# Kernel optimization log

Hardware: AMD Instinct MI355X
Metric: run time of the kernel (lower is better)

## Reference

```python
import jax, jax.numpy as jnp
import numpy as np

EMBED = 1024
HEADS = 16
HEAD = EMBED // HEADS
B, S = 8, 1024


def setup_inputs() -> dict:
    key = jax.random.key(0)
    ks = jax.random.split(key, 12)
    inp = {
        "values": jax.random.normal(ks[0], (B, S, EMBED), jnp.float32),
        "keys": jax.random.normal(ks[1], (B, S, EMBED), jnp.float32),
        "query": jax.random.normal(ks[2], (B, S, EMBED), jnp.float32),
        # causal mask broadcastable to [B, heads, q, k]
        "mask": jnp.broadcast_to(jnp.tril(jnp.ones((S, S), jnp.int32))[None, None], (B, 1, S, S)),
        "Wv": jax.random.normal(ks[3], (HEAD, HEAD), jnp.float32) / np.sqrt(HEAD),
        "bv": jnp.zeros((HEAD,), jnp.float32),
        "Wk": jax.random.normal(ks[4], (HEAD, HEAD), jnp.float32) / np.sqrt(HEAD),
        "bk": jnp.zeros((HEAD,), jnp.float32),
        "Wq": jax.random.normal(ks[5], (HEAD, HEAD), jnp.float32) / np.sqrt(HEAD),
        "bq": jnp.zeros((HEAD,), jnp.float32),
        "Wfc": jax.random.normal(ks[6], (EMBED, EMBED), jnp.float32) / np.sqrt(EMBED),
        "bfc": jnp.zeros((EMBED,), jnp.float32),
    }
    return inp


def reference(values, keys, query, mask, Wv, bv, Wk, bk, Wq, bq, Wfc, bfc):
    N, q_len = query.shape[0], query.shape[1]
    k_len, v_len = keys.shape[1], values.shape[1]
    # split heads: [N, S, H, D]
    v = values.reshape(N, v_len, HEADS, HEAD)
    k = keys.reshape(N, k_len, HEADS, HEAD)
    q = query.reshape(N, q_len, HEADS, HEAD)
    # per-head linear projections (torch Linear: x @ W.T + b)
    v = v @ Wv.T + bv
    k = k @ Wk.T + bk
    q = q @ Wq.T + bq
    # scores [N, H, q, k]
    scores = jnp.einsum('nqhz,nkhz->nhqk', q, k)
    scores = jnp.where(mask == 0, -jnp.inf, scores)
    # NOTE: original divides by sqrt(query_size) (sequence length), not head dim
    attn = jax.nn.softmax(scores / jnp.sqrt(jnp.float32(q_len)), axis=-1)
    out = jnp.einsum('nhqk,nkhz->nqhz', attn, v).reshape(N, q_len, HEADS * HEAD)
    return out @ Wfc.T + bfc
```

## Files before the change

kernel.cpp:

```cpp
#include <hip/hip_runtime.h>
#include <stdint.h>

typedef __attribute__((ext_vector_type(8))) short short8;
typedef __attribute__((ext_vector_type(4))) short short4v;
typedef __attribute__((ext_vector_type(4))) float floatx4;
typedef __attribute__((ext_vector_type(4))) unsigned short ushort4v;

#define HEADS 16
#define HEAD 64
#define SEQ 1024
#define BATCH 8

__device__ __forceinline__ unsigned short f2bf(float f) {
    union { float f; unsigned int u; } v; v.f = f;
    unsigned int r = v.u + 0x7FFFu + ((v.u >> 16) & 1u);
    return (unsigned short)(r >> 16);
}

__device__ __forceinline__ void gload_lds16(const void* g, void* l) {
    __builtin_amdgcn_global_load_lds((const __attribute__((address_space(1))) void*)g,
                                     (__attribute__((address_space(3))) void*)l, 16, 0, 0);
}

__global__ __launch_bounds__(256) void cvt_kernel(const float* __restrict__ in,
                                                  unsigned short* __restrict__ out) {
    int i = (blockIdx.x * 256 + threadIdx.x) * 4;
    float4 f = *(const float4*)(in + i);
    ushort4v v;
    v.x = f2bf(f.x); v.y = f2bf(f.y); v.z = f2bf(f.z); v.w = f2bf(f.w);
    *(ushort4v*)(out + i) = v;
}

__global__ __launch_bounds__(256) void proj_qk_kernel(
    const float* __restrict__ Qin, const float* __restrict__ Kin,
    const float* __restrict__ Wq, const float* __restrict__ bq,
    const float* __restrict__ Wk, const float* __restrict__ bk,
    unsigned short* __restrict__ q_ws, unsigned short* __restrict__ k_ws)
{
    const int tid = threadIdx.x;
    const int wave = tid >> 6, lane = tid & 63;
    const int lq = lane & 15, quad = lane >> 4;
    const int proj = blockIdx.y;

    const float* X = proj ? Kin : Qin;
    const float* W = proj ? Wk : Wq;
    const float* bias = proj ? bk : bq;
    unsigned short* dstb = proj ? k_ws : q_ws;

    const int gr0 = blockIdx.x * 16;
    const int h0 = wave * 4;
    const int b = gr0 >> 10, s0 = gr0 & 1023;

    __shared__ unsigned short sT[4][16 * 68];

    short8 wf[4][2];
#pragma unroll
    for (int nt = 0; nt < 4; ++nt) {
        const float* wr = W + (nt * 16 + lq) * 64 + quad * 8;
#pragma unroll
        for (int ks = 0; ks < 2; ++ks) {
            float4 f0 = *(const float4*)(wr + ks * 32);
            float4 f1 = *(const float4*)(wr + ks * 32 + 4);
            short8 v;
            v[0] = (short)f2bf(f0.x); v[1] = (short)f2bf(f0.y);
            v[2] = (short)f2bf(f0.z); v[3] = (short)f2bf(f0.w);
            v[4] = (short)f2bf(f1.x); v[5] = (short)f2bf(f1.y);
            v[6] = (short)f2bf(f1.z); v[7] = (short)f2bf(f1.w);
            wf[nt][ks] = v;
        }
    }

    float bqk[4];
#pragma unroll
    for (int nt = 0; nt < 4; ++nt) bqk[nt] = bias[nt * 16 + lq];
    const float qscale = 0.03125f * 1.44269504088896340736f;
    const float oscale = proj ? 1.0f : qscale;

    const float* xb = X + (size_t)(gr0 + lq) * 1024 + quad * 8;
    const floatx4 zero4 = {0.f, 0.f, 0.f, 0.f};

    unsigned short* tw = &sT[wave][0];
    const unsigned short* tr = &sT[wave][(lane >> 2) * 68 + (lane & 3) * 16];

    float4 xf[4];
    { const float* p = xb + h0 * 64;
      xf[0] = *(const float4*)p;        xf[1] = *(const float4*)(p + 4);
      xf[2] = *(const float4*)(p + 32); xf[3] = *(const float4*)(p + 36); }
#pragma unroll
    for (int hh = 0; hh < 4; ++hh) {
        float4 xn[4];
        if (hh < 3) {
            const float* p = xb + (h0 + hh + 1) * 64;
            xn[0] = *(const float4*)p;        xn[1] = *(const float4*)(p + 4);
            xn[2] = *(const float4*)(p + 32); xn[3] = *(const float4*)(p + 36);
        }
        short8 aq[2];
#pragma unroll
        for (int ks = 0; ks < 2; ++ks) {
            short8 a;
            a[0] = (short)f2bf(xf[ks * 2].x);     a[1] = (short)f2bf(xf[ks * 2].y);
            a[2] = (short)f2bf(xf[ks * 2].z);     a[3] = (short)f2bf(xf[ks * 2].w);
            a[4] = (short)f2bf(xf[ks * 2 + 1].x); a[5] = (short)f2bf(xf[ks * 2 + 1].y);
            a[6] = (short)f2bf(xf[ks * 2 + 1].z); a[7] = (short)f2bf(xf[ks * 2 + 1].w);
            aq[ks] = a;
        }
        floatx4 acc[4] = {zero4, zero4, zero4, zero4};
#pragma unroll
        for (int ks = 0; ks < 2; ++ks)
#pragma unroll
            for (int nt = 0; nt < 4; ++nt)
                acc[nt] = __builtin_amdgcn_mfma_f32_16x16x32_bf16(aq[ks], wf[nt][ks], acc[nt], 0, 0, 0);

#pragma unroll
        for (int nt = 0; nt < 4; ++nt)
#pragma unroll
            for (int r = 0; r < 4; ++r)
                tw[(quad * 4 + r) * 68 + nt * 16 + lq] = f2bf((acc[nt][r] + bqk[nt]) * oscale);

        short8 o0 = *(const short8*)tr;
        short8 o1 = *(const short8*)(tr + 8);
        unsigned short* dst = dstb + ((size_t)((b * 16 + h0 + hh) * 1024) + s0) * 64 + lane * 16;
        *(short8*)dst = o0;
        *(short8*)(dst + 8) = o1;

#pragma unroll
        for (int i = 0; i < 4; ++i) xf[i] = xn[i];
    }
}

__global__ __launch_bounds__(256) void proj_v_kernel(
    const float* __restrict__ Vin,
    const float* __restrict__ Wv, const float* __restrict__ bv,
    unsigned short* __restrict__ v_ws)
{
    const int tid = threadIdx.x;
    const int wave = tid >> 6, lane = tid & 63;
    const int lq = lane & 15, quad = lane >> 4;

    const int gr0 = blockIdx.x * 16;
    const int h0 = wave * 4;
    const int b = gr0 >> 10, s0 = gr0 & 1023;

    __shared__ unsigned short sT[4][64 * 20];

    short8 wf[4][2];
#pragma unroll
    for (int nt = 0; nt < 4; ++nt) {
        const float* wr = Wv + (nt * 16 + lq) * 64 + quad * 8;
#pragma unroll
        for (int ks = 0; ks < 2; ++ks) {
            float4 f0 = *(const float4*)(wr + ks * 32);
            float4 f1 = *(const float4*)(wr + ks * 32 + 4);
            short8 v;
            v[0] = (short)f2bf(f0.x); v[1] = (short)f2bf(f0.y);
            v[2] = (short)f2bf(f0.z); v[3] = (short)f2bf(f0.w);
            v[4] = (short)f2bf(f1.x); v[5] = (short)f2bf(f1.y);
            v[6] = (short)f2bf(f1.z); v[7] = (short)f2bf(f1.w);
            wf[nt][ks] = v;
        }
    }

    float bvr[4][4];
#pragma unroll
    for (int nt = 0; nt < 4; ++nt)
#pragma unroll
        for (int r = 0; r < 4; ++r) bvr[nt][r] = bv[nt * 16 + quad * 4 + r];

    const float* xb = Vin + (size_t)(gr0 + lq) * 1024 + quad * 8;
    const floatx4 zero4 = {0.f, 0.f, 0.f, 0.f};

    unsigned short* tw = &sT[wave][0];
    const int rrow = lane >> 1, rhalf = lane & 1;
    const unsigned short* tr0 = &sT[wave][rrow * 20 + rhalf * 8];
    const unsigned short* tr1 = &sT[wave][(rrow + 32) * 20 + rhalf * 8];

    float4 xf[4];
    { const float* p = xb + h0 * 64;
      xf[0] = *(const float4*)p;        xf[1] = *(const float4*)(p + 4);
      xf[2] = *(const float4*)(p + 32); xf[3] = *(const float4*)(p + 36); }
#pragma unroll
    for (int hh = 0; hh < 4; ++hh) {
        float4 xn[4];
        if (hh < 3) {
            const float* p = xb + (h0 + hh + 1) * 64;
            xn[0] = *(const float4*)p;        xn[1] = *(const float4*)(p + 4);
            xn[2] = *(const float4*)(p + 32); xn[3] = *(const float4*)(p + 36);
        }
        short8 aq[2];
#pragma unroll
        for (int ks = 0; ks < 2; ++ks) {
            short8 a;
            a[0] = (short)f2bf(xf[ks * 2].x);     a[1] = (short)f2bf(xf[ks * 2].y);
            a[2] = (short)f2bf(xf[ks * 2].z);     a[3] = (short)f2bf(xf[ks * 2].w);
            a[4] = (short)f2bf(xf[ks * 2 + 1].x); a[5] = (short)f2bf(xf[ks * 2 + 1].y);
            a[6] = (short)f2bf(xf[ks * 2 + 1].z); a[7] = (short)f2bf(xf[ks * 2 + 1].w);
            aq[ks] = a;
        }
        floatx4 acc[4] = {zero4, zero4, zero4, zero4};
#pragma unroll
        for (int ks = 0; ks < 2; ++ks)
#pragma unroll
            for (int nt = 0; nt < 4; ++nt)
                acc[nt] = __builtin_amdgcn_mfma_f32_16x16x32_bf16(wf[nt][ks], aq[ks], acc[nt], 0, 0, 0);

#pragma unroll
        for (int nt = 0; nt < 4; ++nt)
#pragma unroll
            for (int r = 0; r < 4; ++r)
                tw[(nt * 16 + quad * 4 + r) * 20 + lq] = f2bf(acc[nt][r] + bvr[nt][r]);

        short8 o0 = *(const short8*)tr0;
        short8 o1 = *(const short8*)tr1;
        unsigned short* vh = v_ws + (size_t)((b * 16 + h0 + hh) * 64) * 1024 + s0 + rhalf * 8;
        *(short8*)(vh + (size_t)rrow * 1024) = o0;
        *(short8*)(vh + (size_t)(rrow + 32) * 1024) = o1;

#pragma unroll
        for (int i = 0; i < 4; ++i) xf[i] = xn[i];
    }
}

__global__ __launch_bounds__(256, 2) void attn_kernel(
    const unsigned short* __restrict__ q_ws, const unsigned short* __restrict__ k_ws,
    const unsigned short* __restrict__ v_ws, unsigned short* __restrict__ attn_ws)
{
    const int bh = blockIdx.x;
    const int b = bh >> 4, h = bh & 15;
    const int tid = threadIdx.x;
    const int wave = tid >> 6, lane = tid & 63;
    const int lq = lane & 15, quad = lane >> 4;
    const int r8 = lane >> 3, ch = lane & 7;
    const int sw = ch ^ r8;

    __shared__ unsigned short sK[64 * 64];
    __shared__ unsigned short sV[64 * 64];
    __shared__ unsigned short sP[4][32 * 64];

    const size_t head_off = (size_t)bh * SEQ * HEAD;
    const unsigned short* qb = q_ws + head_off;
    const unsigned short* kb = k_ws + head_off;
    const unsigned short* vb = v_ws + head_off;

    short8 ones;
#pragma unroll
    for (int j = 0; j < 8; ++j) ones[j] = (short)0x3F80;

    const floatx4 zero4 = {0.f, 0.f, 0.f, 0.f};

    for (int pass = 0; pass < 2; ++pass) {
        const int qt = pass ? (7 - blockIdx.y) : blockIdx.y;
        const int q0 = qt * 128;
        const int q_lo = q0 + wave * 32;
        const int q_hi = q_lo + 31;
        const int nkt = 2 * qt + 2;

        short8 aq[2][2];
#pragma unroll
        for (int rg = 0; rg < 2; ++rg) {
            const unsigned short* qp = qb + (size_t)(q0 + wave * 32 + rg * 16 + lq) * 64 + quad * 8;
            aq[rg][0] = *(const short8*)qp;
            aq[rg][1] = *(const short8*)(qp + 32);
        }

        floatx4 o[2][4];
        floatx4 lacc[2] = {zero4, zero4};
#pragma unroll
        for (int rg = 0; rg < 2; ++rg)
#pragma unroll
            for (int nt = 0; nt < 4; ++nt) o[rg][nt] = zero4;

        for (int kt = 0; kt < nkt; ++kt) {
#pragma unroll
            for (int i = 0; i < 2; ++i) {
                int br = wave * 16 + i * 8;
                const char* gK = (const char*)(kb + (size_t)(kt * 64 + br + r8) * 64) + sw * 16;
                gload_lds16(gK, (char*)sK + br * 128);
                const char* gV = (const char*)(vb + (size_t)(br + r8) * 1024 + kt * 64) + sw * 16;
                gload_lds16(gV, (char*)sV + br * 128);
            }
            __syncthreads();

            const bool skip = (kt * 64 > q_hi);
            if (!skip) {
                const bool full = (kt * 64 + 63 <= q_lo);

                floatx4 s[2][4];
#pragma unroll
                for (int rg = 0; rg < 2; ++rg)
#pragma unroll
                    for (int nt = 0; nt < 4; ++nt) s[rg][nt] = zero4;
#pragma unroll
                for (int ks = 0; ks < 2; ++ks) {
#pragma unroll
                    for (int nt = 0; nt < 4; ++nt) {
                        short8 kf = *(const short8*)(sK + (nt * 16 + lq) * 64 +
                                                     (((quad + 4 * ks) ^ (lq & 7)) * 8));
                        s[0][nt] = __builtin_amdgcn_mfma_f32_16x16x32_bf16(aq[0][ks], kf, s[0][nt], 0, 0, 0);
                        s[1][nt] = __builtin_amdgcn_mfma_f32_16x16x32_bf16(aq[1][ks], kf, s[1][nt], 0, 0, 0);
                    }
                }

                unsigned short* wp = &sP[wave][0];
#pragma unroll
                for (int rg = 0; rg < 2; ++rg) {
#pragma unroll
                    for (int nt = 0; nt < 4; ++nt) {
                        int kcol = kt * 64 + nt * 16 + lq;
                        int chn = (((nt * 2 + (lq >> 3)) ^ (quad << 1)) * 8) + (lq & 7);
#pragma unroll
                        for (int r = 0; r < 4; ++r) {
                            float p = __builtin_amdgcn_exp2f(s[rg][nt][r]);
                            if (!full) {
                                int qrow = q_lo + rg * 16 + quad * 4 + r;
                                if (kcol > qrow) p = 0.f;
                            }
                            wp[(rg * 16 + quad * 4 + r) * 64 + chn] = f2bf(p);
                        }
                    }
                }

                short8 vf[4][2];
#pragma unroll
                for (int nt = 0; nt < 4; ++nt)
#pragma unroll
                    for (int ks = 0; ks < 2; ++ks)
                        vf[nt][ks] = *(const short8*)(sV + (nt * 16 + lq) * 64 +
                                                      (((quad + 4 * ks) ^ (lq & 7)) * 8));
#pragma unroll
                for (int rg = 0; rg < 2; ++rg) {
#pragma unroll
                    for (int ks = 0; ks < 2; ++ks) {
                        short8 pa = *(const short8*)&sP[wave][(rg * 16 + lq) * 64 +
                                     (((ks * 4 + quad) ^ (((lq >> 2) & 3) << 1)) * 8)];
                        lacc[rg] = __builtin_amdgcn_mfma_f32_16x16x32_bf16(pa, ones, lacc[rg], 0, 0, 0);
#pragma unroll
                        for (int nt = 0; nt < 4; ++nt)
                            o[rg][nt] = __builtin_amdgcn_mfma_f32_16x16x32_bf16(pa, vf[nt][ks], o[rg][nt], 0, 0, 0);
                    }
                }
            }
            __syncthreads();
        }

#pragma unroll
        for (int rg = 0; rg < 2; ++rg) {
            float inv[4];
#pragma unroll
            for (int r = 0; r < 4; ++r) inv[r] = 1.f / lacc[rg][r];
            const int srow_base = q0 + wave * 32 + rg * 16 + quad * 4;
#pragma unroll
            for (int nt = 0; nt < 4; ++nt) {
                int col = h * 64 + nt * 16 + lq;
#pragma unroll
                for (int r = 0; r < 4; ++r) {
                    attn_ws[((size_t)(b * SEQ + srow_base + r)) * 1024 + col] = f2bf(o[rg][nt][r] * inv[r]);
                }
            }
        }
    }
}

__global__ __launch_bounds__(256) void fc_kernel(
    const unsigned short* __restrict__ A, const unsigned short* __restrict__ Bw,
    const float* __restrict__ bias, float* __restrict__ out)
{
    const int nt0 = blockIdx.x * 128;
    const int mt0 = blockIdx.y * 128;
    const int tid = threadIdx.x;
    const int wave = tid >> 6, lane = tid & 63;
    const int lq = lane & 15, quad = lane >> 4;
    const int wm = (wave >> 1) * 64, wn = (wave & 1) * 64;

    __shared__ unsigned short sA[128 * 32];
    __shared__ unsigned short sB[128 * 32];

    const floatx4 zero4 = {0.f, 0.f, 0.f, 0.f};
    floatx4 acc[4][4];
#pragma unroll
    for (int i = 0; i < 4; ++i)
#pragma unroll
        for (int j = 0; j < 4; ++j) acc[i][j] = zero4;

    for (int kt = 0; kt < 32; ++kt) {
#pragma unroll
        for (int issue = 0; issue < 2; ++issue) {
            int off = (issue * 4 + wave) * 1024 + lane * 16;
            int row = off >> 6;
            int cb = off & 63;
            const char* ga = (const char*)A + (size_t)(mt0 + row) * 2048 + kt * 64 + cb;
            gload_lds16(ga, (char*)sA + (issue * 4 + wave) * 1024);
            const char* gb = (const char*)Bw + (size_t)(nt0 + row) * 2048 + kt * 64 + cb;
            gload_lds16(gb, (char*)sB + (issue * 4 + wave) * 1024);
        }
        __syncthreads();

        short8 af[4], bf[4];
#pragma unroll
        for (int i = 0; i < 4; ++i) {
            af[i] = *(const short8*)(sA + (wm + i * 16 + lq) * 32 + quad * 8);
            bf[i] = *(const short8*)(sB + (wn + i * 16 + lq) * 32 + quad * 8);
        }
#pragma unroll
        for (int mi = 0; mi < 4; ++mi)
#pragma unroll
            for (int ni = 0; ni < 4; ++ni)
                acc[mi][ni] = __builtin_amdgcn_mfma_f32_16x16x32_bf16(af[mi], bf[ni], acc[mi][ni], 0, 0, 0);
        __syncthreads();
    }

#pragma unroll
    for (int mi = 0; mi < 4; ++mi) {
#pragma unroll
        for (int ni = 0; ni < 4; ++ni) {
            int col = nt0 + wn + ni * 16 + lq;
            float bc = bias[col];
#pragma unroll
            for (int r = 0; r < 4; ++r) {
                int row = mt0 + wm + mi * 16 + quad * 4 + r;
                out[(size_t)row * 1024 + col] = acc[mi][ni][r] + bc;
            }
        }
    }
}

extern "C" void kernel_launch(void* const* d_in, const int* in_sizes, int n_in,
                              void* d_out, int out_size, void* d_ws, size_t ws_size,
                              hipStream_t stream)
{
    const float* values = (const float*)d_in[0];
    const float* keys   = (const float*)d_in[1];
    const float* query  = (const float*)d_in[2];
    const float* Wv  = (const float*)d_in[4];
    const float* bv  = (const float*)d_in[5];
    const float* Wk  = (const float*)d_in[6];
    const float* bk  = (const float*)d_in[7];
    const float* Wq  = (const float*)d_in[8];
    const float* bq  = (const float*)d_in[9];
    const float* Wfc = (const float*)d_in[10];
    const float* bfc = (const float*)d_in[11];
    float* out = (float*)d_out;

    char* ws = (char*)d_ws;
    unsigned short* q_ws    = (unsigned short*)(ws);
    unsigned short* k_ws    = (unsigned short*)(ws + (16u << 20));
    unsigned short* v_ws    = (unsigned short*)(ws + (32u << 20));
    unsigned short* attn_ws = (unsigned short*)(ws + (48u << 20));
    unsigned short* wfc_ws  = (unsigned short*)(ws + (64u << 20));

    cvt_kernel<<<dim3(1024), dim3(256), 0, stream>>>(Wfc, wfc_ws);
    proj_qk_kernel<<<dim3(512, 2), dim3(256), 0, stream>>>(
        query, keys, Wq, bq, Wk, bk, q_ws, k_ws);
    proj_v_kernel<<<dim3(512), dim3(256), 0, stream>>>(values, Wv, bv, v_ws);
    attn_kernel<<<dim3(128, 4), dim3(256), 0, stream>>>(q_ws, k_ws, v_ws, attn_ws);
    fc_kernel<<<dim3(8, 64), dim3(256), 0, stream>>>(attn_ws, wfc_ws, bfc, out);
}
```

Before: 262.6 us.

## Fuse Wfc conversion into V projection, split attention grid, deepen FC K-tile

Folds the Wfc fp32-to-bf16 conversion into proj_v_kernel, which removes one kernel launch. The attention kernel drops its two-pass balanced q-tile pairing in favour of one q-tile per block on an 8-wide grid, and raises the launch-bounds occupancy hint to 4. The FC GEMM moves to a 64-wide K tile with an XOR-swizzled LDS layout, which halves the number of loop iterations and barriers. The risks are causal load imbalance across attention blocks and extra register pressure from the higher occupancy target.

```diff
diff --git a/kernel.cpp b/kernel.cpp
--- a/kernel.cpp
+++ b/kernel.cpp
@@ -2,7 +2,6 @@
 #include <stdint.h>
 
 typedef __attribute__((ext_vector_type(8))) short short8;
-typedef __attribute__((ext_vector_type(4))) short short4v;
 typedef __attribute__((ext_vector_type(4))) float floatx4;
 typedef __attribute__((ext_vector_type(4))) unsigned short ushort4v;
 
@@ -20,15 +19,6 @@
 __device__ __forceinline__ void gload_lds16(const void* g, void* l) {
     __builtin_amdgcn_global_load_lds((const __attribute__((address_space(1))) void*)g,
                                      (__attribute__((address_space(3))) void*)l, 16, 0, 0);
-}
-
-__global__ __launch_bounds__(256) void cvt_kernel(const float* __restrict__ in,
-                                                  unsigned short* __restrict__ out) {
-    int i = (blockIdx.x * 256 + threadIdx.x) * 4;
-    float4 f = *(const float4*)(in + i);
-    ushort4v v;
-    v.x = f2bf(f.x); v.y = f2bf(f.y); v.z = f2bf(f.z); v.w = f2bf(f.w);
-    *(ushort4v*)(out + i) = v;
 }
 
 __global__ __launch_bounds__(256) void proj_qk_kernel(
@@ -131,11 +121,23 @@
 __global__ __launch_bounds__(256) void proj_v_kernel(
     const float* __restrict__ Vin,
     const float* __restrict__ Wv, const float* __restrict__ bv,
+    const float* __restrict__ Wfc, unsigned short* __restrict__ wfc_ws,
     unsigned short* __restrict__ v_ws)
 {
     const int tid = threadIdx.x;
     const int wave = tid >> 6, lane = tid & 63;
     const int lq = lane & 15, quad = lane >> 4;
+
+    {
+        int base = blockIdx.x * 2048 + tid * 8;
+        float4 f0 = *(const float4*)(Wfc + base);
+        float4 f1 = *(const float4*)(Wfc + base + 4);
+        ushort4v v0, v1;
+        v0.x = f2bf(f0.x); v0.y = f2bf(f0.y); v0.z = f2bf(f0.z); v0.w = f2bf(f0.w);
+        v1.x = f2bf(f1.x); v1.y = f2bf(f1.y); v1.z = f2bf(f1.z); v1.w = f2bf(f1.w);
+        *(ushort4v*)(wfc_ws + base) = v0;
+        *(ushort4v*)(wfc_ws + base + 4) = v1;
+    }
 
     const int gr0 = blockIdx.x * 16;
     const int h0 = wave * 4;
@@ -220,7 +222,7 @@
     }
 }
 
-__global__ __launch_bounds__(256, 2) void attn_kernel(
+__global__ __launch_bounds__(256, 4) void attn_kernel(
     const unsigned short* __restrict__ q_ws, const unsigned short* __restrict__ k_ws,
     const unsigned short* __restrict__ v_ws, unsigned short* __restrict__ attn_ws)
 {
@@ -247,114 +249,112 @@
 
     const floatx4 zero4 = {0.f, 0.f, 0.f, 0.f};
 
-    for (int pass = 0; pass < 2; ++pass) {
-        const int qt = pass ? (7 - blockIdx.y) : blockIdx.y;
-        const int q0 = qt * 128;
-        const int q_lo = q0 + wave * 32;
-        const int q_hi = q_lo + 31;
-        const int nkt = 2 * qt + 2;
-
-        short8 aq[2][2];
-#pragma unroll
-        for (int rg = 0; rg < 2; ++rg) {
-            const unsigned short* qp = qb + (size_t)(q0 + wave * 32 + rg * 16 + lq) * 64 + quad * 8;
-            aq[rg][0] = *(const short8*)qp;
-            aq[rg][1] = *(const short8*)(qp + 32);
-        }
-
-        floatx4 o[2][4];
-        floatx4 lacc[2] = {zero4, zero4};
-#pragma unroll
-        for (int rg = 0; rg < 2; ++rg)
-#pragma unroll
-            for (int nt = 0; nt < 4; ++nt) o[rg][nt] = zero4;
-
-        for (int kt = 0; kt < nkt; ++kt) {
-#pragma unroll
-            for (int i = 0; i < 2; ++i) {
-                int br = wave * 16 + i * 8;
-                const char* gK = (const char*)(kb + (size_t)(kt * 64 + br + r8) * 64) + sw * 16;
-                gload_lds16(gK, (char*)sK + br * 128);
-                const char* gV = (const char*)(vb + (size_t)(br + r8) * 1024 + kt * 64) + sw * 16;
-                gload_lds16(gV, (char*)sV + br * 128);
-            }
-            __syncthreads();
-
-            const bool skip = (kt * 64 > q_hi);
-            if (!skip) {
-                const bool full = (kt * 64 + 63 <= q_lo);
-
-                floatx4 s[2][4];
-#pragma unroll
-                for (int rg = 0; rg < 2; ++rg)
-#pragma unroll
-                    for (int nt = 0; nt < 4; ++nt) s[rg][nt] = zero4;
-#pragma unroll
-                for (int ks = 0; ks < 2; ++ks) {
-#pragma unroll
-                    for (int nt = 0; nt < 4; ++nt) {
-                        short8 kf = *(const short8*)(sK + (nt * 16 + lq) * 64 +
-                                                     (((quad + 4 * ks) ^ (lq & 7)) * 8));
-                        s[0][nt] = __builtin_amdgcn_mfma_f32_16x16x32_bf16(aq[0][ks], kf, s[0][nt], 0, 0, 0);
-                        s[1][nt] = __builtin_amdgcn_mfma_f32_16x16x32_bf16(aq[1][ks], kf, s[1][nt], 0, 0, 0);
+    const int qt = blockIdx.y;
+    const int q0 = qt * 128;
+    const int q_lo = q0 + wave * 32;
+    const int q_hi = q_lo + 31;
+    const int nkt = 2 * qt + 2;
+
+    short8 aq[2][2];
+#pragma unroll
+    for (int rg = 0; rg < 2; ++rg) {
+        const unsigned short* qp = qb + (size_t)(q0 + wave * 32 + rg * 16 + lq) * 64 + quad * 8;
+        aq[rg][0] = *(const short8*)qp;
+        aq[rg][1] = *(const short8*)(qp + 32);
+    }
+
+    floatx4 o[2][4];
+    floatx4 lacc[2] = {zero4, zero4};
+#pragma unroll
+    for (int rg = 0; rg < 2; ++rg)
+#pragma unroll
+        for (int nt = 0; nt < 4; ++nt) o[rg][nt] = zero4;
+
+    for (int kt = 0; kt < nkt; ++kt) {
+#pragma unroll
+        for (int i = 0; i < 2; ++i) {
+            int br = wave * 16 + i * 8;
+            const char* gK = (const char*)(kb + (size_t)(kt * 64 + br + r8) * 64) + sw * 16;
+            gload_lds16(gK, (char*)sK + br * 128);
+            const char* gV = (const char*)(vb + (size_t)(br + r8) * 1024 + kt * 64) + sw * 16;
+            gload_lds16(gV, (char*)sV + br * 128);
+        }
+        __syncthreads();
+
+        const bool skip = (kt * 64 > q_hi);
+        if (!skip) {
+            const bool full = (kt * 64 + 63 <= q_lo);
+
+            floatx4 s[2][4];
+#pragma unroll
+            for (int rg = 0; rg < 2; ++rg)
+#pragma unroll
+                for (int nt = 0; nt < 4; ++nt) s[rg][nt] = zero4;
+#pragma unroll
+            for (int ks = 0; ks < 2; ++ks) {
+#pragma unroll
+                for (int nt = 0; nt < 4; ++nt) {
+                    short8 kf = *(const short8*)(sK + (nt * 16 + lq) * 64 +
+                                                 (((quad + 4 * ks) ^ (lq & 7)) * 8));
+                    s[0][nt] = __builtin_amdgcn_mfma_f32_16x16x32_bf16(aq[0][ks], kf, s[0][nt], 0, 0, 0);
+                    s[1][nt] = __builtin_amdgcn_mfma_f32_16x16x32_bf16(aq[1][ks], kf, s[1][nt], 0, 0, 0);
+                }
+            }
+
+            unsigned short* wp = &sP[wave][0];
+#pragma unroll
+            for (int rg = 0; rg < 2; ++rg) {
+#pragma unroll
+                for (int nt = 0; nt < 4; ++nt) {
+                    int kcol = kt * 64 + nt * 16 + lq;
+                    int chn = (((nt * 2 + (lq >> 3)) ^ (quad << 1)) * 8) + (lq & 7);
+#pragma unroll
+                    for (int r = 0; r < 4; ++r) {
+                        float p = __builtin_amdgcn_exp2f(s[rg][nt][r]);
+                        if (!full) {
+                            int qrow = q_lo + rg * 16 + quad * 4 + r;
+                            if (kcol > qrow) p = 0.f;
+                        }
+                        wp[(rg * 16 + quad * 4 + r) * 64 + chn] = f2bf(p);
                     }
                 }
-
-                unsigned short* wp = &sP[wave][0];
-#pragma unroll
-                for (int rg = 0; rg < 2; ++rg) {
-#pragma unroll
-                    for (int nt = 0; nt < 4; ++nt) {
-                        int kcol = kt * 64 + nt * 16 + lq;
-                        int chn = (((nt * 2 + (lq >> 3)) ^ (quad << 1)) * 8) + (lq & 7);
-#pragma unroll
-                        for (int r = 0; r < 4; ++r) {
-                            float p = __builtin_amdgcn_exp2f(s[rg][nt][r]);
-                            if (!full) {
-                                int qrow = q_lo + rg * 16 + quad * 4 + r;
-                                if (kcol > qrow) p = 0.f;
-                            }
-                            wp[(rg * 16 + quad * 4 + r) * 64 + chn] = f2bf(p);
-                        }
-                    }
+            }
+
+            short8 vf[4][2];
+#pragma unroll
+            for (int nt = 0; nt < 4; ++nt)
+#pragma unroll
+                for (int ks = 0; ks < 2; ++ks)
+                    vf[nt][ks] = *(const short8*)(sV + (nt * 16 + lq) * 64 +
+                                                  (((quad + 4 * ks) ^ (lq & 7)) * 8));
+#pragma unroll
+            for (int rg = 0; rg < 2; ++rg) {
+#pragma unroll
+                for (int ks = 0; ks < 2; ++ks) {
+                    short8 pa = *(const short8*)&sP[wave][(rg * 16 + lq) * 64 +
+                                 (((ks * 4 + quad) ^ (((lq >> 2) & 3) << 1)) * 8)];
+                    lacc[rg] = __builtin_amdgcn_mfma_f32_16x16x32_bf16(pa, ones, lacc[rg], 0, 0, 0);
+#pragma unroll
+                    for (int nt = 0; nt < 4; ++nt)
+                        o[rg][nt] = __builtin_amdgcn_mfma_f32_16x16x32_bf16(pa, vf[nt][ks], o[rg][nt], 0, 0, 0);
                 }
-
-                short8 vf[4][2];
-#pragma unroll
-                for (int nt = 0; nt < 4; ++nt)
-#pragma unroll
-                    for (int ks = 0; ks < 2; ++ks)
-                        vf[nt][ks] = *(const short8*)(sV + (nt * 16 + lq) * 64 +
-                                                      (((quad + 4 * ks) ^ (lq & 7)) * 8));
-#pragma unroll
-                for (int rg = 0; rg < 2; ++rg) {
-#pragma unroll
-                    for (int ks = 0; ks < 2; ++ks) {
-                        short8 pa = *(const short8*)&sP[wave][(rg * 16 + lq) * 64 +
-                                     (((ks * 4 + quad) ^ (((lq >> 2) & 3) << 1)) * 8)];
-                        lacc[rg] = __builtin_amdgcn_mfma_f32_16x16x32_bf16(pa, ones, lacc[rg], 0, 0, 0);
-#pragma unroll
-                        for (int nt = 0; nt < 4; ++nt)
-                            o[rg][nt] = __builtin_amdgcn_mfma_f32_16x16x32_bf16(pa, vf[nt][ks], o[rg][nt], 0, 0, 0);
-                    }
-                }
-            }
-            __syncthreads();
-        }
-
-#pragma unroll
-        for (int rg = 0; rg < 2; ++rg) {
-            float inv[4];
-#pragma unroll
-            for (int r = 0; r < 4; ++r) inv[r] = 1.f / lacc[rg][r];
-            const int srow_base = q0 + wave * 32 + rg * 16 + quad * 4;
-#pragma unroll
-            for (int nt = 0; nt < 4; ++nt) {
-                int col = h * 64 + nt * 16 + lq;
-#pragma unroll
-                for (int r = 0; r < 4; ++r) {
-                    attn_ws[((size_t)(b * SEQ + srow_base + r)) * 1024 + col] = f2bf(o[rg][nt][r] * inv[r]);
-                }
+            }
+        }
+        __syncthreads();
+    }
+
+#pragma unroll
+    for (int rg = 0; rg < 2; ++rg) {
+        float inv[4];
+#pragma unroll
+        for (int r = 0; r < 4; ++r) inv[r] = 1.f / lacc[rg][r];
+        const int srow_base = q0 + wave * 32 + rg * 16 + quad * 4;
+#pragma unroll
+        for (int nt = 0; nt < 4; ++nt) {
+            int col = h * 64 + nt * 16 + lq;
+#pragma unroll
+            for (int r = 0; r < 4; ++r) {
+                attn_ws[((size_t)(b * SEQ + srow_base + r)) * 1024 + col] = f2bf(o[rg][nt][r] * inv[r]);
             }
         }
     }
@@ -371,8 +371,8 @@
     const int lq = lane & 15, quad = lane >> 4;
     const int wm = (wave >> 1) * 64, wn = (wave & 1) * 64;
 
-    __shared__ unsigned short sA[128 * 32];
-    __shared__ unsigned short sB[128 * 32];
+    __shared__ unsigned short sA[128 * 64];
+    __shared__ unsigned short sB[128 * 64];
 
     const floatx4 zero4 = {0.f, 0.f, 0.f, 0.f};
     floatx4 acc[4][4];
@@ -381,30 +381,37 @@
 #pragma unroll
         for (int j = 0; j < 4; ++j) acc[i][j] = zero4;
 
-    for (int kt = 0; kt < 32; ++kt) {
-#pragma unroll
-        for (int issue = 0; issue < 2; ++issue) {
-            int off = (issue * 4 + wave) * 1024 + lane * 16;
-            int row = off >> 6;
-            int cb = off & 63;
-            const char* ga = (const char*)A + (size_t)(mt0 + row) * 2048 + kt * 64 + cb;
-            gload_lds16(ga, (char*)sA + (issue * 4 + wave) * 1024);
-            const char* gb = (const char*)Bw + (size_t)(nt0 + row) * 2048 + kt * 64 + cb;
-            gload_lds16(gb, (char*)sB + (issue * 4 + wave) * 1024);
+    const int sc = (tid & 7) ^ ((tid >> 3) & 7);
+    const int sr = tid >> 3;
+
+    for (int kt = 0; kt < 16; ++kt) {
+#pragma unroll
+        for (int j = 0; j < 4; ++j) {
+            int r = j * 32 + sr;
+            const char* ga = (const char*)A + (size_t)(mt0 + r) * 2048 + kt * 128 + sc * 16;
+            gload_lds16(ga, (char*)sA + (j * 256 + tid) * 16);
+            const char* gb = (const char*)Bw + (size_t)(nt0 + r) * 2048 + kt * 128 + sc * 16;
+            gload_lds16(gb, (char*)sB + (j * 256 + tid) * 16);
         }
         __syncthreads();
 
-        short8 af[4], bf[4];
-#pragma unroll
-        for (int i = 0; i < 4; ++i) {
-            af[i] = *(const short8*)(sA + (wm + i * 16 + lq) * 32 + quad * 8);
-            bf[i] = *(const short8*)(sB + (wn + i * 16 + lq) * 32 + quad * 8);
-        }
-#pragma unroll
-        for (int mi = 0; mi < 4; ++mi)
-#pragma unroll
-            for (int ni = 0; ni < 4; ++ni)
-                acc[mi][ni] = __builtin_amdgcn_mfma_f32_16x16x32_bf16(af[mi], bf[ni], acc[mi][ni], 0, 0, 0);
+        short8 af[4][2], bf[4][2];
+#pragma unroll
+        for (int i = 0; i < 4; ++i)
+#pragma unroll
+            for (int ks = 0; ks < 2; ++ks) {
+                af[i][ks] = *(const short8*)(sA + (wm + i * 16 + lq) * 64 +
+                                             (((quad + 4 * ks) ^ (lq & 7)) * 8));
+                bf[i][ks] = *(const short8*)(sB + (wn + i * 16 + lq) * 64 +
+                                             (((quad + 4 * ks) ^ (lq & 7)) * 8));
+            }
+#pragma unroll
+        for (int ks = 0; ks < 2; ++ks)
+#pragma unroll
+            for (int mi = 0; mi < 4; ++mi)
+#pragma unroll
+                for (int ni = 0; ni < 4; ++ni)
+                    acc[mi][ni] = __builtin_amdgcn_mfma_f32_16x16x32_bf16(af[mi][ks], bf[ni][ks], acc[mi][ni], 0, 0, 0);
         __syncthreads();
     }
 
@@ -447,10 +454,9 @@
     unsigned short* attn_ws = (unsigned short*)(ws + (48u << 20));
     unsigned short* wfc_ws  = (unsigned short*)(ws + (64u << 20));
 
-    cvt_kernel<<<dim3(1024), dim3(256), 0, stream>>>(Wfc, wfc_ws);
     proj_qk_kernel<<<dim3(512, 2), dim3(256), 0, stream>>>(
         query, keys, Wq, bq, Wk, bk, q_ws, k_ws);
-    proj_v_kernel<<<dim3(512), dim3(256), 0, stream>>>(values, Wv, bv, v_ws);
-    attn_kernel<<<dim3(128, 4), dim3(256), 0, stream>>>(q_ws, k_ws, v_ws, attn_ws);
+    proj_v_kernel<<<dim3(512), dim3(256), 0, stream>>>(values, Wv, bv, Wfc, wfc_ws, v_ws);
+    attn_kernel<<<dim3(128, 8), dim3(256), 0, stream>>>(q_ws, k_ws, v_ws, attn_ws);
     fc_kernel<<<dim3(8, 64), dim3(256), 0, stream>>>(attn_ws, wfc_ws, bfc, out);
 }
```

After: 256.8 us. -2.2%, faster.
